# Kernel optimization log

Measured on AMD Instinct MI355X. Metric: run time of the kernel, lower is better.

Reference implementation:

```python
import jax, jax.numpy as jnp
import numpy as np

DIM = 512
HEADS = 8
DIM_HEAD = 64  # default dim_head used for scale, matches DIM//HEADS here
SCALE = DIM_HEAD ** -0.5
B, X, Y = 8, 32, 32


def setup_inputs() -> dict:
    key = jax.random.key(0)
    k0, k1, k2, k3 = jax.random.split(key, 4)
    fmap = jax.random.normal(k0, (B, DIM, X, Y), dtype=jnp.float32)
    # 1x1 convs as matrices: weight [out, in]
    Wqkvl = jax.random.normal(k1, (4 * DIM, DIM), dtype=jnp.float32) * (DIM ** -0.5)
    Wout = jax.random.normal(k2, (DIM, DIM), dtype=jnp.float32) * (DIM ** -0.5)
    bout = jax.random.normal(k3, (DIM,), dtype=jnp.float32) * 0.01
    return {"fmap": fmap, "Wqkvl": Wqkvl, "Wout": Wout, "bout": bout}


def reference(fmap, Wqkvl, Wout, bout):
    b, c, x, y = fmap.shape
    h, d = HEADS, c // HEADS
    n = x * y
    # 1x1 conv projection to q,k,v,L
    qkvL = jnp.einsum('oc,bcxy->boxy', Wqkvl, fmap)  # [b, 4c, x, y]
    q, k, v, L = jnp.split(qkvL, 4, axis=1)
    # 'b (h d) x y -> b h (x y) d'
    def to_tokens(t):
        return t.reshape(b, h, d, n).transpose(0, 1, 3, 2)
    q, k, v, L = map(to_tokens, (q, k, v, L))
    dots = jnp.einsum('bhid,bhjd->bhij', q, k) * SCALE  # [b,h,n,n]
    attn = jax.nn.softmax(dots, axis=-1)
    out = jnp.einsum('bhij,bhjd->bhid', attn, v) + L  # [b,h,n,d]
    # 'b h (x y) d -> b (h d) x y'
    out = out.transpose(0, 1, 3, 2).reshape(b, c, x, y)
    # output 1x1 conv with bias (dropout=0 -> identity)
    out = jnp.einsum('oc,bcxy->boxy', Wout, out) + bout[None, :, None, None]
    return out
```

## Files before the change

### kernel.cpp

```cpp
#include <hip/hip_runtime.h>

#define Bn 8
#define Cn 512
#define Hn 8
#define Dn 64
#define Nn 1024
#define SCALEQ 0.125f

typedef unsigned short u16;
typedef unsigned short u16x8 __attribute__((ext_vector_type(8)));
typedef unsigned short u16x4 __attribute__((ext_vector_type(4)));
typedef short s16x4 __attribute__((ext_vector_type(4)));
typedef float f32x4 __attribute__((ext_vector_type(4)));
typedef __bf16 bf16x8 __attribute__((ext_vector_type(8)));

__device__ __forceinline__ u16 f2bf(float f){
  unsigned u = __float_as_uint(f);
  u += 0x7fffu + ((u >> 16) & 1u);
  return (u16)(u >> 16);
}
__device__ __forceinline__ float bf2f(u16 h){
  return __uint_as_float(((unsigned)h) << 16);
}
__device__ __forceinline__ f32x4 mfma16(u16x8 a, u16x8 b, f32x4 c){
  return __builtin_amdgcn_mfma_f32_16x16x32_bf16(
      __builtin_bit_cast(bf16x8, a), __builtin_bit_cast(bf16x8, b), c, 0, 0, 0);
}
__device__ __forceinline__ f32x4 mfma16k16(u16x4 a, u16x4 b, f32x4 c){
  return __builtin_amdgcn_mfma_f32_16x16x16bf16_1k(
      __builtin_bit_cast(s16x4, a), __builtin_bit_cast(s16x4, b), c, 0, 0, 0);
}

__device__ __forceinline__ void gload16(const u16* src, u16* dst){
  __builtin_amdgcn_global_load_lds(
      (const __attribute__((address_space(1))) unsigned int*)src,
      (__attribute__((address_space(3))) unsigned int*)dst, 16, 0, 0);
}

__global__ __launch_bounds__(256) void k_convert2(const float* __restrict__ s1,
                                                  const float* __restrict__ s2,
                                                  u16* __restrict__ d1, u16* __restrict__ d2,
                                                  int n1, int n2){
  int i = blockIdx.x * 256 + threadIdx.x;
  const float* s; u16* d; int j;
  if (i < n1){ s = s1; d = d1; j = i; }
  else { if (i >= n1 + n2) return; s = s2; d = d2; j = i - n1; }
  float4 f = reinterpret_cast<const float4*>(s)[j];
  u16x4 o;
  o[0] = f2bf(f.x); o[1] = f2bf(f.y); o[2] = f2bf(f.z); o[3] = f2bf(f.w);
  reinterpret_cast<u16x4*>(d)[j] = o;
}

__global__ __launch_bounds__(256) void k_transpose(const float* __restrict__ fmap,
                                                   u16* __restrict__ fmapT){
  __shared__ float tile[32][33];
  const int n0 = blockIdx.x * 32, c0 = blockIdx.y * 32, b = blockIdx.z;
  const int tx = threadIdx.x & 31, ty = threadIdx.x >> 5;
  const float* src = fmap + ((size_t)b * Cn + c0) * Nn + n0;
#pragma unroll
  for (int i = 0; i < 4; i++) tile[ty + 8*i][tx] = src[(size_t)(ty + 8*i) * Nn + tx];
  __syncthreads();
  u16* dst = fmapT + ((size_t)b * Nn + n0) * Cn + c0;
#pragma unroll
  for (int i = 0; i < 4; i++) dst[(size_t)(ty + 8*i) * Cn + tx] = f2bf(tile[tx][ty + 8*i]);
}

__device__ __forceinline__ void stage64(const u16* g, size_t ldg, u16* lbase, int w, int lane){
#pragma unroll
  for (int s = 0; s < 2; s++){
    int row = s*32 + w*8 + (lane>>3);
    const u16* src = g + (size_t)row*ldg + (((lane&7) ^ (row&7)) * 8);
    u16* dst = lbase + (s*32 + w*8)*64;
    gload16(src, dst);
  }
}
__device__ __forceinline__ void stage128x32(const u16* g, size_t ldg, u16* lbase, int w, int lane){
#pragma unroll
  for (int s = 0; s < 2; s++){
    int row = s*64 + w*16 + (lane>>2);
    const u16* src = g + (size_t)row*ldg + (((lane&3) ^ (row&3)) * 8);
    u16* dst = lbase + (s*64 + w*16)*32;
    gload16(src, dst);
  }
}

__device__ __forceinline__ void gemm_fma(const u16x8 (&af)[4], const u16x8 (&bf)[4],
                                         f32x4 (&acc)[4][4]){
#pragma unroll
  for (int i = 0; i < 4; i++)
#pragma unroll
    for (int j = 0; j < 4; j++)
      acc[i][j] = mfma16(af[i], bf[j], acc[i][j]);
}

__device__ __forceinline__ void gemm_nt_128(const u16* __restrict__ Ap, int lda,
                                            const u16* __restrict__ Bp, int ldb,
                                            u16* sA, u16* sB,
                                            f32x4 (&acc)[4][4]){
  const int tid = threadIdx.x;
  const int w = tid >> 6, lane = tid & 63, r = lane & 15, g = lane >> 4;
  const int wi = w >> 1, wj = w & 1;
  stage128x32(Ap, lda, sA, w, lane);
  stage128x32(Bp, ldb, sB, w, lane);
  for (int ks = 0; ks < Cn/32; ks++){
    __syncthreads();
    const int cur = ks & 1;
    if (ks + 1 < Cn/32){
      stage128x32(Ap + (ks+1)*32, lda, sA + (cur^1)*128*32, w, lane);
      stage128x32(Bp + (ks+1)*32, ldb, sB + (cur^1)*128*32, w, lane);
    }
    const u16* Al = sA + cur*128*32;
    const u16* Bl = sB + cur*128*32;
    u16x8 af[4], bf[4];
#pragma unroll
    for (int t = 0; t < 4; t++){
      int ar = wi*64 + t*16 + r;
      af[t] = *reinterpret_cast<const u16x8*>(&Al[ar*32 + ((g ^ (ar&3)) * 8)]);
      int br = wj*64 + t*16 + r;
      bf[t] = *reinterpret_cast<const u16x8*>(&Bl[br*32 + ((g ^ (br&3)) * 8)]);
    }
    gemm_fma(af, bf, acc);
  }
}

__global__ __launch_bounds__(256) void k_gemm1(const u16* __restrict__ fmapT,
                                               const u16* __restrict__ W1,
                                               u16* __restrict__ Qb, u16* __restrict__ Kb,
                                               u16* __restrict__ Vt, u16* __restrict__ Lb){
  __shared__ u16 sA[2*128*32], sB[2*128*32];
  const int ob = blockIdx.x;
  const int nb = blockIdx.y;
  const int b  = blockIdx.z;
  const int w = threadIdx.x >> 6, wi = w >> 1, wj = w & 1;
  const int lane = threadIdx.x & 63, r = lane & 15, g = lane >> 4;
  const int seg = ob >> 2;

  f32x4 acc[4][4];
  const f32x4 z = {0.f, 0.f, 0.f, 0.f};
#pragma unroll
  for (int i = 0; i < 4; i++)
#pragma unroll
    for (int j = 0; j < 4; j++) acc[i][j] = z;

  const u16* fbase = fmapT + (size_t)b * Nn * Cn;

  if (seg != 2){
    gemm_nt_128(fbase + (size_t)(nb*128) * Cn, Cn, W1 + (size_t)(ob*128) * Cn, Cn, sA, sB, acc);
    u16* dst = (seg == 0) ? Qb : (seg == 1 ? Kb : Lb);
    const float sc = (seg == 0) ? SCALEQ : 1.0f;
#pragma unroll
    for (int it = 0; it < 4; it++)
#pragma unroll
      for (int jt = 0; jt < 4; jt++)
#pragma unroll
        for (int rr = 0; rr < 4; rr++){
          int n = nb*128 + wi*64 + it*16 + 4*g + rr;
          int o = ob*128 + wj*64 + jt*16 + r;
          dst[((size_t)b * Nn + n) * Cn + (o & 511)] = f2bf(acc[it][jt][rr] * sc);
        }
  } else {
    gemm_nt_128(W1 + (size_t)(ob*128) * Cn, Cn, fbase + (size_t)(nb*128) * Cn, Cn, sA, sB, acc);
#pragma unroll
    for (int it = 0; it < 4; it++)
#pragma unroll
      for (int jt = 0; jt < 4; jt++)
#pragma unroll
        for (int rr = 0; rr < 4; rr++){
          int o = ob*128 + wi*64 + it*16 + 4*g + rr;
          int oo = o - 1024;
          int h = oo >> 6, d = oo & 63;
          int n = nb*128 + wj*64 + jt*16 + r;
          Vt[(((size_t)b * Hn + h) * Dn + d) * Nn + n] = f2bf(acc[it][jt][rr]);
        }
  }
}

__device__ __forceinline__ void attn_tile(const u16* Kc, const u16* Vc,
                                          const u16* kbase, const u16* vbase, int next,
                                          u16* Kn, u16* Vn,
                                          int w, int lane, int r, int g,
                                          u16x8 qA0, u16x8 qA1, u16x8 qB0, u16x8 qB1,
                                          float& mA, float& mB,
                                          f32x4 (&accA)[4], f32x4 (&accB)[4],
                                          f32x4& accSA, f32x4& accSB){
  const f32x4 z = {0.f, 0.f, 0.f, 0.f};
  __syncthreads();
  if (next < 16){
    stage64(kbase + (size_t)next*64*Cn, Cn, Kn, w, lane);
    stage64(vbase + next*64,            Nn, Vn, w, lane);
  }
  f32x4 sA[4], sB[4];
#pragma unroll
  for (int t = 0; t < 4; t++){
    int row = 16*t + r;
    u16x8 k0 = *reinterpret_cast<const u16x8*>(&Kc[row*64 + ((g       ^ (r&7)) * 8)]);
    u16x8 k1 = *reinterpret_cast<const u16x8*>(&Kc[row*64 + (((4+g)   ^ (r&7)) * 8)]);
    sA[t] = mfma16(k0, qA0, z); sA[t] = mfma16(k1, qA1, sA[t]);
    sB[t] = mfma16(k0, qB0, z); sB[t] = mfma16(k1, qB1, sB[t]);
  }
  float tmA = -1e30f, tmB = -1e30f;
#pragma unroll
  for (int t = 0; t < 4; t++){
    tmA = fmaxf(tmA, fmaxf(fmaxf(sA[t][0], sA[t][1]), fmaxf(sA[t][2], sA[t][3])));
    tmB = fmaxf(tmB, fmaxf(fmaxf(sB[t][0], sB[t][1]), fmaxf(sB[t][2], sB[t][3])));
  }
  tmA = fmaxf(tmA, __shfl_xor(tmA, 16)); tmA = fmaxf(tmA, __shfl_xor(tmA, 32));
  tmB = fmaxf(tmB, __shfl_xor(tmB, 16)); tmB = fmaxf(tmB, __shfl_xor(tmB, 32));
  if (__any(tmA - mA > 8.f)){
    float mn = fmaxf(mA, tmA), al = __expf(mA - mn);
    mA = mn; accSA *= al;
#pragma unroll
    for (int dt = 0; dt < 4; dt++) accA[dt] *= al;
  }
  if (__any(tmB - mB > 8.f)){
    float mn = fmaxf(mB, tmB), al = __expf(mB - mn);
    mB = mn; accSB *= al;
#pragma unroll
    for (int dt = 0; dt < 4; dt++) accB[dt] *= al;
  }
  u16x4 pA[4], pB[4];
#pragma unroll
  for (int t = 0; t < 4; t++){
#pragma unroll
    for (int j = 0; j < 4; j++){
      pA[t][j] = __builtin_bit_cast(u16, (__bf16)__expf(sA[t][j] - mA));
      pB[t][j] = __builtin_bit_cast(u16, (__bf16)__expf(sB[t][j] - mB));
    }
  }
  const u16x4 ones = {0x3F80u, 0x3F80u, 0x3F80u, 0x3F80u};
#pragma unroll
  for (int t = 0; t < 4; t++){
    accSA = mfma16k16(ones, pA[t], accSA);
    accSB = mfma16k16(ones, pB[t], accSB);
  }
#pragma unroll
  for (int s = 0; s < 4; s++)
#pragma unroll
    for (int dt = 0; dt < 4; dt++){
      int row = dt*16 + r;
      u16x4 vf = *reinterpret_cast<const u16x4*>(
          &Vc[row*64 + (((2*s + (g>>1)) ^ (r&7)) * 8) + (g&1)*4]);
      accA[dt] = mfma16k16(vf, pA[s], accA[dt]);
      accB[dt] = mfma16k16(vf, pB[s], accB[dt]);
    }
}

__global__ __launch_bounds__(256, 2) void k_attn(const u16* __restrict__ Qb,
                                                 const u16* __restrict__ Kb,
                                                 const u16* __restrict__ Vt,
                                                 const u16* __restrict__ Lb,
                                                 u16* __restrict__ tok){
  __shared__ u16 Kl[2*64*64], Vl[2*64*64];
  const int bid = blockIdx.x;
  const int w0 = (bid & 7) * 64 + (bid >> 3);
  const int qblk = w0 & 7, h = (w0 >> 3) & 7, b = w0 >> 6;
  const int w = threadIdx.x >> 6, lane = threadIdx.x & 63;
  const int r = lane & 15, g = lane >> 4;
  const int qA = qblk * 128 + w * 16;
  const int qB = qA + 64;

  const u16* qrowA = Qb + ((size_t)b * Nn + qA + r) * Cn + h * Dn + 8 * g;
  const u16* qrowB = Qb + ((size_t)b * Nn + qB + r) * Cn + h * Dn + 8 * g;
  u16x8 qA0 = *reinterpret_cast<const u16x8*>(qrowA);
  u16x8 qA1 = *reinterpret_cast<const u16x8*>(qrowA + 32);
  u16x8 qB0 = *reinterpret_cast<const u16x8*>(qrowB);
  u16x8 qB1 = *reinterpret_cast<const u16x8*>(qrowB + 32);

  const u16* kbase = Kb + (size_t)b * Nn * Cn + h * Dn;
  const u16* vbase = Vt + ((size_t)b * Hn + h) * Dn * Nn;

  f32x4 accA[4], accB[4];
  const f32x4 z = {0.f, 0.f, 0.f, 0.f};
#pragma unroll
  for (int dt = 0; dt < 4; dt++){ accA[dt] = z; accB[dt] = z; }
  f32x4 accSA = z, accSB = z;
  float mA = -1e30f, mB = -1e30f;

  u16* Kl0 = Kl, *Kl1 = Kl + 64*64;
  u16* Vl0 = Vl, *Vl1 = Vl + 64*64;
  stage64(kbase, Cn, Kl0, w, lane);
  stage64(vbase, Nn, Vl0, w, lane);

  for (int tile = 0; tile < 16; tile += 2){
    attn_tile(Kl0, Vl0, kbase, vbase, tile + 1, Kl1, Vl1, w, lane, r, g,
              qA0, qA1, qB0, qB1, mA, mB, accA, accB, accSA, accSB);
    attn_tile(Kl1, Vl1, kbase, vbase, tile + 2, Kl0, Vl0, w, lane, r, g,
              qA0, qA1, qB0, qB1, mA, mB, accA, accB, accSA, accSB);
  }

  float linvA = 1.0f / accSA[0];
  float linvB = 1.0f / accSB[0];
#pragma unroll
  for (int half = 0; half < 2; half++){
    const int n = (half ? qB : qA) + r;
    const float linv = half ? linvB : linvA;
    const f32x4* acc = half ? accB : accA;
    const u16* lrow = Lb + ((size_t)b * Nn + n) * Cn + h * Dn;
    u16* trow = tok + ((size_t)b * Nn + n) * Cn + h * Dn;
#pragma unroll
    for (int dt = 0; dt < 4; dt++){
      u16x4 lv = *reinterpret_cast<const u16x4*>(lrow + dt*16 + 4*g);
      u16x4 ov;
#pragma unroll
      for (int rr = 0; rr < 4; rr++)
        ov[rr] = f2bf(acc[dt][rr] * linv + bf2f(lv[rr]));
      *reinterpret_cast<u16x4*>(trow + dt*16 + 4*g) = ov;
    }
  }
}

__global__ __launch_bounds__(256) void k_gemm2(const u16* __restrict__ tok,
                                               const u16* __restrict__ Wo,
                                               const float* __restrict__ bout,
                                               float* __restrict__ out){
  __shared__ u16 sA[2*128*32], sB[2*128*32];
  const int ob = blockIdx.x;
  const int nb = blockIdx.y;
  const int b  = blockIdx.z;
  const int w = threadIdx.x >> 6, wi = w >> 1, wj = w & 1;
  const int lane = threadIdx.x & 63, r = lane & 15, g = lane >> 4;

  f32x4 acc[4][4];
  const f32x4 z = {0.f, 0.f, 0.f, 0.f};
#pragma unroll
  for (int i = 0; i < 4; i++)
#pragma unroll
    for (int j = 0; j < 4; j++) acc[i][j] = z;

  gemm_nt_128(Wo + (size_t)(ob*128) * Cn, Cn,
              tok + (size_t)b * Nn * Cn + (size_t)(nb*128) * Cn, Cn, sA, sB, acc);

#pragma unroll
  for (int it = 0; it < 4; it++)
#pragma unroll
    for (int jt = 0; jt < 4; jt++)
#pragma unroll
      for (int rr = 0; rr < 4; rr++){
        int o = ob*128 + wi*64 + it*16 + 4*g + rr;
        int n = nb*128 + wj*64 + jt*16 + r;
        out[((size_t)b * Cn + o) * Nn + n] = acc[it][jt][rr] + bout[o];
      }
}

extern "C" void kernel_launch(void* const* d_in, const int* in_sizes, int n_in,
                              void* d_out, int out_size, void* d_ws, size_t ws_size,
                              hipStream_t stream){
  const float* fmap  = (const float*)d_in[0];
  const float* Wqkvl = (const float*)d_in[1];
  const float* Wout  = (const float*)d_in[2];
  const float* bout  = (const float*)d_in[3];
  float* out = (float*)d_out;

  char* ws = (char*)d_ws;
  size_t off = 0;
  auto alloc = [&](size_t bytes) -> void* {
    void* p = ws + off;
    off += (bytes + 255) & ~(size_t)255;
    return p;
  };
  u16* W1bf  = (u16*)alloc((size_t)4*Cn*Cn*2);
  u16* Wobf  = (u16*)alloc((size_t)Cn*Cn*2);
  u16* fmapT = (u16*)alloc((size_t)Bn*Nn*Cn*2);
  u16* Qb    = (u16*)alloc((size_t)Bn*Nn*Cn*2);
  u16* Kb    = (u16*)alloc((size_t)Bn*Nn*Cn*2);
  u16* Lb    = (u16*)alloc((size_t)Bn*Nn*Cn*2);
  u16* Vt    = (u16*)alloc((size_t)Bn*Hn*Dn*Nn*2);
  u16* tok   = fmapT;

  const int n1 = 4*Cn*Cn/4, n2 = Cn*Cn/4;
  hipLaunchKernelGGL(k_convert2, dim3((n1 + n2 + 255)/256), dim3(256), 0, stream,
                     Wqkvl, Wout, W1bf, Wobf, n1, n2);
  hipLaunchKernelGGL(k_transpose, dim3(Nn/32, Cn/32, Bn), dim3(256), 0, stream, fmap, fmapT);
  hipLaunchKernelGGL(k_gemm1, dim3(16, 8, Bn), dim3(256), 0, stream, fmapT, W1bf, Qb, Kb, Vt, Lb);
  hipLaunchKernelGGL(k_attn, dim3(512), dim3(256), 0, stream, Qb, Kb, Vt, Lb, tok);
  hipLaunchKernelGGL(k_gemm2, dim3(4, 8, Bn), dim3(256), 0, stream, tok, Wobf, bout, out);
}
```

Before: 90.29 us.

## Widen attention KV tiles, vectorize transpose stores, remap GEMM blocks per XCD

The attention kernel now stages K/V tiles of 128 keys instead of 64, halving the loop trips and barriers per block at the cost of doubled LDS and more live score registers. The transpose kernel handles 64 channels per block and writes 16-byte bf16 vectors instead of scalar stores. Both projection GEMMs switch to a 1D grid with an XCD-aware block remap so that neighbouring tiles that share inputs land on the same chiplet's L2. Higher register and LDS use may lower occupancy in the attention kernel.

```diff
diff --git a/kernel.cpp b/kernel.cpp
--- a/kernel.cpp
+++ b/kernel.cpp
@@ -53,34 +53,40 @@
 
 __global__ __launch_bounds__(256) void k_transpose(const float* __restrict__ fmap,
                                                    u16* __restrict__ fmapT){
-  __shared__ float tile[32][33];
-  const int n0 = blockIdx.x * 32, c0 = blockIdx.y * 32, b = blockIdx.z;
+  __shared__ float tile[64][33];
+  const int n0 = blockIdx.x * 32, c0 = blockIdx.y * 64, b = blockIdx.z;
   const int tx = threadIdx.x & 31, ty = threadIdx.x >> 5;
   const float* src = fmap + ((size_t)b * Cn + c0) * Nn + n0;
 #pragma unroll
-  for (int i = 0; i < 4; i++) tile[ty + 8*i][tx] = src[(size_t)(ty + 8*i) * Nn + tx];
+  for (int i = 0; i < 8; i++) tile[ty + 8*i][tx] = src[(size_t)(ty + 8*i) * Nn + tx];
   __syncthreads();
-  u16* dst = fmapT + ((size_t)b * Nn + n0) * Cn + c0;
-#pragma unroll
-  for (int i = 0; i < 4; i++) dst[(size_t)(ty + 8*i) * Cn + tx] = f2bf(tile[tx][ty + 8*i]);
-}
-
-__device__ __forceinline__ void stage64(const u16* g, size_t ldg, u16* lbase, int w, int lane){
-#pragma unroll
-  for (int s = 0; s < 2; s++){
+  const int nr = threadIdx.x >> 3;
+  const int cj = (threadIdx.x & 7) * 8;
+  u16x8 o;
+#pragma unroll
+  for (int k = 0; k < 8; k++) o[k] = f2bf(tile[cj + k][nr]);
+  *reinterpret_cast<u16x8*>(fmapT + ((size_t)b * Nn + n0 + nr) * Cn + c0 + cj) = o;
+}
+
+__device__ __forceinline__ void stageK(const u16* g, u16* lbase, int w, int lane){
+#pragma unroll
+  for (int s = 0; s < 4; s++){
     int row = s*32 + w*8 + (lane>>3);
-    const u16* src = g + (size_t)row*ldg + (((lane&7) ^ (row&7)) * 8);
-    u16* dst = lbase + (s*32 + w*8)*64;
-    gload16(src, dst);
+    gload16(g + (size_t)row*Cn + (((lane&7) ^ (row&7)) * 8), lbase + (s*32 + w*8)*64);
+  }
+}
+__device__ __forceinline__ void stageV(const u16* g, u16* lbase, int w, int lane){
+#pragma unroll
+  for (int s = 0; s < 4; s++){
+    int row = s*16 + w*4 + (lane>>4);
+    gload16(g + (size_t)row*Nn + (((lane&15) ^ (row&7)) * 8), lbase + (s*16 + w*4)*128);
   }
 }
 __device__ __forceinline__ void stage128x32(const u16* g, size_t ldg, u16* lbase, int w, int lane){
 #pragma unroll
   for (int s = 0; s < 2; s++){
     int row = s*64 + w*16 + (lane>>2);
-    const u16* src = g + (size_t)row*ldg + (((lane&3) ^ (row&3)) * 8);
-    u16* dst = lbase + (s*64 + w*16)*32;
-    gload16(src, dst);
+    gload16(g + (size_t)row*ldg + (((lane&3) ^ (row&3)) * 8), lbase + (s*64 + w*16)*32);
   }
 }
 
@@ -128,9 +134,9 @@
                                                u16* __restrict__ Qb, u16* __restrict__ Kb,
                                                u16* __restrict__ Vt, u16* __restrict__ Lb){
   __shared__ u16 sA[2*128*32], sB[2*128*32];
-  const int ob = blockIdx.x;
-  const int nb = blockIdx.y;
-  const int b  = blockIdx.z;
+  const int lin = blockIdx.x;
+  const int wid = (lin & 7) * 128 + (lin >> 3);
+  const int ob = wid & 15, nb = (wid >> 4) & 7, b = wid >> 7;
   const int w = threadIdx.x >> 6, wi = w >> 1, wj = w & 1;
   const int lane = threadIdx.x & 63, r = lane & 15, g = lane >> 4;
   const int seg = ob >> 2;
@@ -185,22 +191,22 @@
                                           f32x4& accSA, f32x4& accSB){
   const f32x4 z = {0.f, 0.f, 0.f, 0.f};
   __syncthreads();
-  if (next < 16){
-    stage64(kbase + (size_t)next*64*Cn, Cn, Kn, w, lane);
-    stage64(vbase + next*64,            Nn, Vn, w, lane);
-  }
-  f32x4 sA[4], sB[4];
-#pragma unroll
-  for (int t = 0; t < 4; t++){
+  if (next < 8){
+    stageK(kbase + (size_t)next*128*Cn, Kn, w, lane);
+    stageV(vbase + next*128,            Vn, w, lane);
+  }
+  f32x4 sA[8], sB[8];
+#pragma unroll
+  for (int t = 0; t < 8; t++){
     int row = 16*t + r;
-    u16x8 k0 = *reinterpret_cast<const u16x8*>(&Kc[row*64 + ((g       ^ (r&7)) * 8)]);
-    u16x8 k1 = *reinterpret_cast<const u16x8*>(&Kc[row*64 + (((4+g)   ^ (r&7)) * 8)]);
+    u16x8 k0 = *reinterpret_cast<const u16x8*>(&Kc[row*64 + ((g     ^ (r&7)) * 8)]);
+    u16x8 k1 = *reinterpret_cast<const u16x8*>(&Kc[row*64 + (((4+g) ^ (r&7)) * 8)]);
     sA[t] = mfma16(k0, qA0, z); sA[t] = mfma16(k1, qA1, sA[t]);
     sB[t] = mfma16(k0, qB0, z); sB[t] = mfma16(k1, qB1, sB[t]);
   }
   float tmA = -1e30f, tmB = -1e30f;
 #pragma unroll
-  for (int t = 0; t < 4; t++){
+  for (int t = 0; t < 8; t++){
     tmA = fmaxf(tmA, fmaxf(fmaxf(sA[t][0], sA[t][1]), fmaxf(sA[t][2], sA[t][3])));
     tmB = fmaxf(tmB, fmaxf(fmaxf(sB[t][0], sB[t][1]), fmaxf(sB[t][2], sB[t][3])));
   }
@@ -218,9 +224,9 @@
 #pragma unroll
     for (int dt = 0; dt < 4; dt++) accB[dt] *= al;
   }
-  u16x4 pA[4], pB[4];
-#pragma unroll
-  for (int t = 0; t < 4; t++){
+  u16x4 pA[8], pB[8];
+#pragma unroll
+  for (int t = 0; t < 8; t++){
 #pragma unroll
     for (int j = 0; j < 4; j++){
       pA[t][j] = __builtin_bit_cast(u16, (__bf16)__expf(sA[t][j] - mA));
@@ -229,17 +235,17 @@
   }
   const u16x4 ones = {0x3F80u, 0x3F80u, 0x3F80u, 0x3F80u};
 #pragma unroll
-  for (int t = 0; t < 4; t++){
+  for (int t = 0; t < 8; t++){
     accSA = mfma16k16(ones, pA[t], accSA);
     accSB = mfma16k16(ones, pB[t], accSB);
   }
 #pragma unroll
-  for (int s = 0; s < 4; s++)
+  for (int s = 0; s < 8; s++)
 #pragma unroll
     for (int dt = 0; dt < 4; dt++){
       int row = dt*16 + r;
       u16x4 vf = *reinterpret_cast<const u16x4*>(
-          &Vc[row*64 + (((2*s + (g>>1)) ^ (r&7)) * 8) + (g&1)*4]);
+          &Vc[row*128 + (((2*s + (g>>1)) ^ (r&7)) * 8) + (g&1)*4]);
       accA[dt] = mfma16k16(vf, pA[s], accA[dt]);
       accB[dt] = mfma16k16(vf, pB[s], accB[dt]);
     }
@@ -250,7 +256,7 @@
                                                  const u16* __restrict__ Vt,
                                                  const u16* __restrict__ Lb,
                                                  u16* __restrict__ tok){
-  __shared__ u16 Kl[2*64*64], Vl[2*64*64];
+  __shared__ u16 Kl[2*128*64], Vl[2*64*128];
   const int bid = blockIdx.x;
   const int w0 = (bid & 7) * 64 + (bid >> 3);
   const int qblk = w0 & 7, h = (w0 >> 3) & 7, b = w0 >> 6;
@@ -276,12 +282,12 @@
   f32x4 accSA = z, accSB = z;
   float mA = -1e30f, mB = -1e30f;
 
-  u16* Kl0 = Kl, *Kl1 = Kl + 64*64;
-  u16* Vl0 = Vl, *Vl1 = Vl + 64*64;
-  stage64(kbase, Cn, Kl0, w, lane);
-  stage64(vbase, Nn, Vl0, w, lane);
-
-  for (int tile = 0; tile < 16; tile += 2){
+  u16* Kl0 = Kl, *Kl1 = Kl + 128*64;
+  u16* Vl0 = Vl, *Vl1 = Vl + 64*128;
+  stageK(kbase, Kl0, w, lane);
+  stageV(vbase, Vl0, w, lane);
+
+  for (int tile = 0; tile < 8; tile += 2){
     attn_tile(Kl0, Vl0, kbase, vbase, tile + 1, Kl1, Vl1, w, lane, r, g,
               qA0, qA1, qB0, qB1, mA, mB, accA, accB, accSA, accSB);
     attn_tile(Kl1, Vl1, kbase, vbase, tile + 2, Kl0, Vl0, w, lane, r, g,
@@ -314,9 +320,9 @@
                                                const float* __restrict__ bout,
                                                float* __restrict__ out){
   __shared__ u16 sA[2*128*32], sB[2*128*32];
-  const int ob = blockIdx.x;
-  const int nb = blockIdx.y;
-  const int b  = blockIdx.z;
+  const int lin = blockIdx.x;
+  const int wid = (lin & 7) * 32 + (lin >> 3);
+  const int ob = wid & 3, nb = (wid >> 2) & 7, b = wid >> 5;
   const int w = threadIdx.x >> 6, wi = w >> 1, wj = w & 1;
   const int lane = threadIdx.x & 63, r = lane & 15, g = lane >> 4;
 
@@ -370,8 +376,8 @@
   const int n1 = 4*Cn*Cn/4, n2 = Cn*Cn/4;
   hipLaunchKernelGGL(k_convert2, dim3((n1 + n2 + 255)/256), dim3(256), 0, stream,
                      Wqkvl, Wout, W1bf, Wobf, n1, n2);
-  hipLaunchKernelGGL(k_transpose, dim3(Nn/32, Cn/32, Bn), dim3(256), 0, stream, fmap, fmapT);
-  hipLaunchKernelGGL(k_gemm1, dim3(16, 8, Bn), dim3(256), 0, stream, fmapT, W1bf, Qb, Kb, Vt, Lb);
+  hipLaunchKernelGGL(k_transpose, dim3(Nn/32, Cn/64, Bn), dim3(256), 0, stream, fmap, fmapT);
+  hipLaunchKernelGGL(k_gemm1, dim3(1024), dim3(256), 0, stream, fmapT, W1bf, Qb, Kb, Vt, Lb);
   hipLaunchKernelGGL(k_attn, dim3(512), dim3(256), 0, stream, Qb, Kb, Vt, Lb, tok);
-  hipLaunchKernelGGL(k_gemm2, dim3(4, 8, Bn), dim3(256), 0, stream, tok, Wobf, bout, out);
-}
+  hipLaunchKernelGGL(k_gemm2, dim3(256), dim3(256), 0, stream, tok, Wobf, bout, out);
+}
```

Measured after the change: 90.11 us. About the same (-0.2%).
